# Optimization experiments

Measured on AMD Instinct MI355X. Metric: run time of the kernel, lower is better.

## Reference

```python
import jax, jax.numpy as jnp
import numpy as np

N = 50000
E = 800000
IN_C = 128
HID = 128
OUT_C = 128
EPS = 1e-5


def _glorot(key, shape):
    fan_in = shape[-1]
    return jax.random.normal(key, shape, dtype=jnp.float32) / jnp.sqrt(jnp.float32(fan_in))


def setup_inputs() -> dict:
    key = jax.random.key(0)
    ks = jax.random.split(key, 16)
    inp = {
        'x': jax.random.normal(ks[0], (N, IN_C), dtype=jnp.float32),
        'edge_index': jax.random.randint(ks[1], (2, E), 0, N, dtype=jnp.int64),
    }
    dims = [(IN_C, HID), (HID, HID), (HID, OUT_C)]
    for i, (din, dout) in enumerate(dims, start=1):
        inp[f'Wl{i}'] = _glorot(ks[2 * i], (dout, din))      # applied to aggregated neighbors
        inp[f'bl{i}'] = jnp.zeros((dout,), dtype=jnp.float32)
        inp[f'Wr{i}'] = _glorot(ks[2 * i + 1], (dout, din))  # applied to root node
        inp[f'g{i}'] = jnp.ones((dout,), dtype=jnp.float32)   # BN gamma
        inp[f'b{i}'] = jnp.zeros((dout,), dtype=jnp.float32)  # BN beta
    inp['Wlin'] = _glorot(ks[10], (OUT_C, 2 * HID + OUT_C))
    inp['blin'] = jnp.zeros((OUT_C,), dtype=jnp.float32)
    return inp


def _sage(x, src, dst, Wl, bl, Wr):
    # mean aggregation of source features at target nodes (PyG SAGEConv default)
    msg = x[src]                                              # [E, C]
    s = jax.ops.segment_sum(msg, dst, num_segments=N)         # [N, C]
    cnt = jax.ops.segment_sum(jnp.ones((src.shape[0], 1), x.dtype), dst, num_segments=N)
    aggr = s / jnp.maximum(cnt, 1.0)
    return aggr @ Wl.T + bl + x @ Wr.T


def _bn(x, g, b):
    # training-mode BatchNorm1d over the node dimension
    mu = jnp.mean(x, axis=0)
    var = jnp.var(x, axis=0)
    return g * (x - mu) * jax.lax.rsqrt(var + EPS) + b


def reference(x, edge_index, Wl1, bl1, Wr1, g1, b1, Wl2, bl2, Wr2, g2, b2,
              Wl3, bl3, Wr3, g3, b3, Wlin, blin):
    src, dst = edge_index[0], edge_index[1]
    x1 = _bn(jax.nn.relu(_sage(x, src, dst, Wl1, bl1, Wr1)), g1, b1)
    x2 = _bn(jax.nn.relu(_sage(x1, src, dst, Wl2, bl2, Wr2)), g2, b2)
    x3 = _bn(jax.nn.relu(_sage(x2, src, dst, Wl3, bl3, Wr3)), g3, b3)
    cat = jnp.concatenate([x1, x2, x3], axis=-1)              # [N, 2*HID + OUT_C]
    return jax.nn.relu(cat @ Wlin.T + blin)
```

## Files before the change

### kernel.cpp

```cpp
#include <hip/hip_runtime.h>

#define NN 50000
#define NE 800000
#define CH 128
#define EPSV 1e-5f

typedef unsigned short ushort_t;
typedef __attribute__((ext_vector_type(8))) short short8_t;
typedef __attribute__((ext_vector_type(8))) unsigned short u16x8;
typedef __attribute__((ext_vector_type(4))) float f32x4;

__device__ inline float bf2f(ushort_t u) {
    union { unsigned int i; float f; } t; t.i = ((unsigned int)u) << 16; return t.f;
}
__device__ inline ushort_t f2bf(float f) {
    union { float f; unsigned int i; } t; t.f = f;
    unsigned int r = t.i + 0x7fff + ((t.i >> 16) & 1);
    return (ushort_t)(r >> 16);
}


__global__ void k_hist(const int* __restrict__ dst, int* __restrict__ deg) {
    int e = blockIdx.x * blockDim.x + threadIdx.x;
    if (e < NE) atomicAdd(&deg[dst[e]], 1);
}

__global__ void k_scan(const int* __restrict__ deg, int* __restrict__ row_ptr) {
    __shared__ int wsum[16];
    const int t = threadIdx.x;
    const int lane = t & 63;
    const int wid = t >> 6;
    int carry = 0;
    for (int base = 0; base < NN; base += 1024) {
        int i = base + t;
        int v = (i < NN) ? deg[i] : 0;
        int x = v;
        #pragma unroll
        for (int off = 1; off < 64; off <<= 1) {
            int y = __shfl_up(x, off, 64);
            if (lane >= off) x += y;
        }
        if (lane == 63) wsum[wid] = x;
        __syncthreads();
        if (wid == 0 && lane < 16) {
            int s = wsum[lane];
            #pragma unroll
            for (int off = 1; off < 16; off <<= 1) {
                int y = __shfl_up(s, off, 16);
                if (lane >= off) s += y;
            }
            wsum[lane] = s;
        }
        __syncthreads();
        int wbase = (wid > 0) ? wsum[wid - 1] : 0;
        if (i < NN) row_ptr[i] = carry + wbase + x - v;
        carry += wsum[15];
        __syncthreads();
    }
    if (t == 0) row_ptr[NN] = carry;
}

__global__ void k_fill(const int* __restrict__ src, const int* __restrict__ dst,
                       const int* __restrict__ row_ptr, int* __restrict__ fillc,
                       int* __restrict__ csr) {
    int e = blockIdx.x * blockDim.x + threadIdx.x;
    if (e < NE) {
        int d = dst[e];
        int pos = row_ptr[d] + atomicAdd(&fillc[d], 1);
        csr[pos] = src[e];
    }
}


__global__ __launch_bounds__(256) void k_cvtX(const float* __restrict__ x,
                                              ushort_t* __restrict__ xb) {
    int i = blockIdx.x * 256 + threadIdx.x;
    if (i >= NN * 32) return;
    float4 v = ((const float4*)x)[i];
    ushort4 o;
    o.x = f2bf(v.x); o.y = f2bf(v.y); o.z = f2bf(v.z); o.w = f2bf(v.w);
    ((ushort4*)xb)[i] = o;
}

__global__ __launch_bounds__(256) void k_pack2(const float* __restrict__ s0,
                                               const float* __restrict__ s1,
                                               ushort_t* __restrict__ dst) {
    int t = blockIdx.x * 256 + threadIdx.x;
    if (t >= 128 * 256) return;
    int o = t >> 8, k = t & 255;
    float v = (k < 128) ? s0[o * 128 + k] : s1[o * 128 + k - 128];
    dst[t] = f2bf(v);
}

__global__ void k_packfold(const float* __restrict__ Wl, const float* __restrict__ Wr,
                           const float* __restrict__ ab, const float* __restrict__ bl,
                           ushort_t* __restrict__ Wp, float* __restrict__ bias) {
    __shared__ float red[128];
    int o = blockIdx.x;
    int k = threadIdx.x;
    float wr = Wr[o * 128 + k];
    Wp[o * 256 + k]       = f2bf(Wl[o * 128 + k]);
    Wp[o * 256 + 128 + k] = f2bf(wr * ab[k]);
    red[k] = wr * ab[128 + k];
    __syncthreads();
    for (int s = 64; s > 0; s >>= 1) {
        if (k < s) red[k] += red[k + s];
        __syncthreads();
    }
    if (k == 0) bias[o] = bl[o] + red[0];
}

__global__ void k_packfoldF(const float* __restrict__ Wlin,
                            const float* __restrict__ ab1, const float* __restrict__ ab2,
                            const float* __restrict__ ab3, const float* __restrict__ blin,
                            ushort_t* __restrict__ Wp, float* __restrict__ bias) {
    __shared__ float red[128];
    int o = blockIdx.x;
    int k = threadIdx.x;
    const float* abs_[3] = {ab1, ab2, ab3};
    float dot = 0.f;
    #pragma unroll
    for (int i = 0; i < 3; ++i) {
        float w = Wlin[o * 384 + i * 128 + k];
        Wp[o * 384 + i * 128 + k] = f2bf(w * abs_[i][k]);
        dot += w * abs_[i][128 + k];
    }
    red[k] = dot;
    __syncthreads();
    for (int s = 64; s > 0; s >>= 1) {
        if (k < s) red[k] += red[k + s];
        __syncthreads();
    }
    if (k == 0) bias[o] = blin[o] + red[0];
}


template<bool FOLD>
__global__ __launch_bounds__(256) void k_aggr(const ushort_t* __restrict__ x,
        const int* __restrict__ row_ptr, const int* __restrict__ csr,
        const float* __restrict__ ab, ushort_t* __restrict__ aggr) {
    const int node = blockIdx.x * 4 + (threadIdx.x >> 6);
    const int lane = threadIdx.x & 63;
    const int l4 = lane & 15;
    const int q  = lane >> 4;
    const int r0 = row_ptr[node], r1 = row_ptr[node + 1];
    const int d = r1 - r0;

    float accA[8] = {0, 0, 0, 0, 0, 0, 0, 0};
    float accB[8] = {0, 0, 0, 0, 0, 0, 0, 0};

    int j = r0 + q;
    for (; j + 4 < r1; j += 8) {
        int s0 = csr[j], s1 = csr[j + 4];
        u16x8 v0 = *(const u16x8*)&x[(size_t)s0 * CH + l4 * 8];
        u16x8 v1 = *(const u16x8*)&x[(size_t)s1 * CH + l4 * 8];
        #pragma unroll
        for (int i = 0; i < 8; ++i) {
            accA[i] += bf2f(v0[i]);
            accB[i] += bf2f(v1[i]);
        }
    }
    for (; j < r1; j += 4) {
        int s0 = csr[j];
        u16x8 v0 = *(const u16x8*)&x[(size_t)s0 * CH + l4 * 8];
        #pragma unroll
        for (int i = 0; i < 8; ++i) accA[i] += bf2f(v0[i]);
    }

    const float sc = d > 0 ? 1.0f / (float)d : 0.0f;
    #pragma unroll
    for (int i = 0; i < 8; ++i) {
        float s = accA[i] + accB[i];
        s += __shfl_xor(s, 16);
        s += __shfl_xor(s, 32);
        accA[i] = s * sc;
    }

    if (q == 0) {
        u16x8 ov;
        #pragma unroll
        for (int i = 0; i < 8; ++i) {
            float v = accA[i];
            if (FOLD) v = d > 0 ? fmaf(v, ab[l4 * 8 + i], ab[128 + l4 * 8 + i]) : 0.f;
            ov[i] = f2bf(v);
        }
        *(u16x8*)&aggr[(size_t)node * CH + l4 * 8] = ov;
    }
}


#define STAGE(buf, t) do {                                                           \
    const ushort_t* Ab_ = (((t) >> 1) == 0) ? A0 : ((((t) >> 1) == 1) ? A1 : A2);    \
    Ab_ += ((t) & 1) * 64;                                                           \
    const ushort_t* Wb_ = W + (t) * 64;                                              \
    _Pragma("unroll")                                                                \
    for (int i_ = 0; i_ < 4; ++i_) {                                                 \
        int f_ = i_ * 256 + tid;                                                     \
        int row_ = f_ >> 3;                                                          \
        int c_ = (f_ & 7) ^ (row_ & 7);                                              \
        int gr_ = bn0 + row_; gr_ = gr_ < NN ? gr_ : NN - 1;                         \
        __builtin_amdgcn_global_load_lds(                                            \
            (const __attribute__((address_space(1))) unsigned int*)(Ab_ + (size_t)gr_ * CH + c_ * 8), \
            (__attribute__((address_space(3))) unsigned int*)(&Abuf[buf][f_ * 8]),   \
            16, 0, 0);                                                               \
        __builtin_amdgcn_global_load_lds(                                            \
            (const __attribute__((address_space(1))) unsigned int*)(Wb_ + (size_t)row_ * (NT * 64) + c_ * 8), \
            (__attribute__((address_space(3))) unsigned int*)(&Wbuf[buf][f_ * 8]),   \
            16, 0, 0);                                                               \
    } } while (0)

template<int NT, bool STATS, bool F32OUT>
__global__ __launch_bounds__(256, 2) void k_mgemm(
    const ushort_t* __restrict__ A0, const ushort_t* __restrict__ A1,
    const ushort_t* __restrict__ A2,
    const ushort_t* __restrict__ W, const float* __restrict__ bias,
    ushort_t* __restrict__ outb, float* __restrict__ outf,
    float* __restrict__ bn_sums)
{
    __shared__ __align__(16) ushort_t Abuf[2][128 * 64];
    __shared__ __align__(16) ushort_t Wbuf[2][128 * 64];
    __shared__ float bns[128], bnq[128];

    const int tid  = threadIdx.x;
    const int lane = tid & 63;
    const int wid  = tid >> 6;
    const int l15  = lane & 15;
    const int lg   = lane >> 4;
    const int wn   = (wid >> 1) * 64;
    const int wo   = (wid & 1) * 64;
    const int bn0  = blockIdx.x * 128;

    if (STATS && tid < 128) { bns[tid] = 0.f; bnq[tid] = 0.f; }

    f32x4 acc[4][4];
    #pragma unroll
    for (int i = 0; i < 4; ++i)
        #pragma unroll
        for (int j = 0; j < 4; ++j)
            acc[i][j] = (f32x4){0.f, 0.f, 0.f, 0.f};

    STAGE(0, 0);
    asm volatile("s_waitcnt vmcnt(0)");
    __syncthreads();

    #pragma unroll
    for (int t = 0; t < NT; ++t) {
        const int cur = t & 1;
        if (t + 1 < NT) STAGE(cur ^ 1, t + 1);
        #pragma unroll
        for (int s = 0; s < 2; ++s) {
            short8_t af[4], wf[4];
            #pragma unroll
            for (int b = 0; b < 4; ++b) {
                int ra = wn + b * 16 + l15;
                int ca = (s * 4 + lg) ^ (ra & 7);
                af[b] = *(const short8_t*)&Abuf[cur][ra * 64 + ca * 8];
                int rw = wo + b * 16 + l15;
                int cw = (s * 4 + lg) ^ (rw & 7);
                wf[b] = *(const short8_t*)&Wbuf[cur][rw * 64 + cw * 8];
            }
            #pragma unroll
            for (int i = 0; i < 4; ++i)
                #pragma unroll
                for (int j = 0; j < 4; ++j)
                    acc[i][j] = __builtin_amdgcn_mfma_f32_16x16x32_bf16(
                        af[i], wf[j], acc[i][j], 0, 0, 0);
        }
        asm volatile("s_waitcnt vmcnt(0)");
        __syncthreads();
    }

    float bv[4];
    #pragma unroll
    for (int j = 0; j < 4; ++j) bv[j] = bias[wo + j * 16 + l15];

    float sum[4] = {0.f, 0.f, 0.f, 0.f}, sq[4] = {0.f, 0.f, 0.f, 0.f};

    #pragma unroll
    for (int i = 0; i < 4; ++i) {
        #pragma unroll
        for (int r = 0; r < 4; ++r) {
            int gn = bn0 + wn + i * 16 + lg * 4 + r;
            bool ok = gn < NN;
            #pragma unroll
            for (int j = 0; j < 4; ++j) {
                int o = wo + j * 16 + l15;
                float v = acc[i][j][r] + bv[j];
                v = fmaxf(v, 0.f);
                if (ok) {
                    if (F32OUT) outf[(size_t)gn * CH + o] = v;
                    else        outb[(size_t)gn * CH + o] = f2bf(v);
                    if (STATS) { sum[j] += v; sq[j] += v * v; }
                }
            }
        }
    }

    if (STATS) {
        #pragma unroll
        for (int j = 0; j < 4; ++j) {
            float ss = sum[j], qq = sq[j];
            ss += __shfl_xor(ss, 16); qq += __shfl_xor(qq, 16);
            ss += __shfl_xor(ss, 32); qq += __shfl_xor(qq, 32);
            if (lg == 0) {
                atomicAdd(&bns[wo + j * 16 + l15], ss);
                atomicAdd(&bnq[wo + j * 16 + l15], qq);
            }
        }
        __syncthreads();
        if (tid < 128) {
            atomicAdd(&bn_sums[tid], bns[tid]);
            atomicAdd(&bn_sums[128 + tid], bnq[tid]);
        }
    }
}


__global__ void k_bnfin(const float* __restrict__ bn_sums, const float* __restrict__ g,
                        const float* __restrict__ b, float* __restrict__ ab) {
    int o = threadIdx.x;
    float mu = bn_sums[o] * (1.0f / NN);
    float var = bn_sums[128 + o] * (1.0f / NN) - mu * mu;
    var = var > 0.f ? var : 0.f;
    float rstd = rsqrtf(var + EPSV);
    float a = g[o] * rstd;
    ab[o] = a;
    ab[128 + o] = b[o] - a * mu;
}


extern "C" void kernel_launch(void* const* d_in, const int* in_sizes, int n_in,
                              void* d_out, int out_size, void* d_ws, size_t ws_size,
                              hipStream_t stream) {
    const float* x  = (const float*)d_in[0];
    const int*   ei = (const int*)d_in[1];
    const int* esrc = ei;
    const int* edst = ei + NE;

    const float* Wl[3] = {(const float*)d_in[2],  (const float*)d_in[7],  (const float*)d_in[12]};
    const float* bl[3] = {(const float*)d_in[3],  (const float*)d_in[8],  (const float*)d_in[13]};
    const float* Wr[3] = {(const float*)d_in[4],  (const float*)d_in[9],  (const float*)d_in[14]};
    const float* gg[3] = {(const float*)d_in[5],  (const float*)d_in[10], (const float*)d_in[15]};
    const float* bb[3] = {(const float*)d_in[6],  (const float*)d_in[11], (const float*)d_in[16]};
    const float* Wlin  = (const float*)d_in[17];
    const float* blin  = (const float*)d_in[18];

    float* fo = (float*)d_out;

    const size_t NC = (size_t)NN * CH;
    ushort_t* xb     = (ushort_t*)d_ws;
    ushort_t* y1b    = xb + NC;
    ushort_t* y2b    = y1b + NC;
    ushort_t* y3b    = y2b + NC;
    ushort_t* aggr_b = y3b + NC;
    ushort_t* Wp1    = aggr_b + NC;
    ushort_t* Wp2    = Wp1 + 128 * 256;
    ushort_t* Wp3    = Wp2 + 128 * 256;
    ushort_t* WpF    = Wp3 + 128 * 256;
    float* bias2     = (float*)(WpF + 128 * 384);
    float* bias3     = bias2 + 128;
    float* biasF     = bias3 + 128;
    float* bn_sums   = biasF + 128;
    float* ab        = bn_sums + 768;
    int* row_ptr     = (int*)(ab + 768);
    int* fillc       = row_ptr + NN + 1;
    int* csr         = fillc + NN;

    hipMemsetAsync(fillc, 0, NN * sizeof(int), stream);
    k_hist<<<(NE + 255) / 256, 256, 0, stream>>>(edst, fillc);
    k_scan<<<1, 1024, 0, stream>>>(fillc, row_ptr);
    hipMemsetAsync(fillc, 0, NN * sizeof(int), stream);
    k_fill<<<(NE + 255) / 256, 256, 0, stream>>>(esrc, edst, row_ptr, fillc, csr);

    k_cvtX<<<(NN * 32 + 255) / 256, 256, 0, stream>>>(x, xb);
    k_pack2<<<128, 256, 0, stream>>>(Wl[0], Wr[0], Wp1);
    hipMemsetAsync(bn_sums, 0, 768 * sizeof(float), stream);

    const int GEMM_GRID = (NN + 127) / 128;

    k_aggr<false><<<NN / 4, 256, 0, stream>>>(xb, row_ptr, csr, nullptr, aggr_b);
    k_mgemm<4, true, false><<<GEMM_GRID, 256, 0, stream>>>(
        aggr_b, xb, nullptr, Wp1, bl[0], y1b, nullptr, bn_sums);
    k_bnfin<<<1, 128, 0, stream>>>(bn_sums, gg[0], bb[0], ab);
    k_packfold<<<128, 128, 0, stream>>>(Wl[1], Wr[1], ab, bl[1], Wp2, bias2);

    k_aggr<true><<<NN / 4, 256, 0, stream>>>(y1b, row_ptr, csr, ab, aggr_b);
    k_mgemm<4, true, false><<<GEMM_GRID, 256, 0, stream>>>(
        aggr_b, y1b, nullptr, Wp2, bias2, y2b, nullptr, bn_sums + 256);
    k_bnfin<<<1, 128, 0, stream>>>(bn_sums + 256, gg[1], bb[1], ab + 256);
    k_packfold<<<128, 128, 0, stream>>>(Wl[2], Wr[2], ab + 256, bl[2], Wp3, bias3);

    k_aggr<true><<<NN / 4, 256, 0, stream>>>(y2b, row_ptr, csr, ab + 256, aggr_b);
    k_mgemm<4, true, false><<<GEMM_GRID, 256, 0, stream>>>(
        aggr_b, y2b, nullptr, Wp3, bias3, y3b, nullptr, bn_sums + 512);
    k_bnfin<<<1, 128, 0, stream>>>(bn_sums + 512, gg[2], bb[2], ab + 512);
    k_packfoldF<<<128, 128, 0, stream>>>(Wlin, ab, ab + 256, ab + 512, blin, WpF, biasF);

    k_mgemm<6, false, true><<<GEMM_GRID, 256, 0, stream>>>(
        y1b, y2b, y3b, WpF, biasF, nullptr, fo, nullptr);
}
```

Measured before the change: 373.3 us.

## Fuse neighbor aggregation into SAGE GEMM and partition CSR build passes

Each SAGE layer's mean aggregation is now computed inside the GEMM kernel: 4 threads per node gather neighbor rows straight into LDS, and the MFMA step then runs over the full K=256 without writing and re-reading an aggr buffer in global memory. The CSR histogram and fill kernels are split into 4 passes over destination ranges, which keeps the atomic targets more cache-local. The tradeoff is a large LDS footprint (one block per CU), a gather phase with less memory parallelism per thread than the old wave-per-node scheme, and four times the reads of the edge list.

```diff
diff --git a/kernel.cpp b/kernel.cpp
--- a/kernel.cpp
+++ b/kernel.cpp
@@ -4,6 +4,8 @@
 #define NE 800000
 #define CH 128
 #define EPSV 1e-5f
+#define NPASS 4
+#define PRANGE 12500
 
 typedef unsigned short ushort_t;
 typedef __attribute__((ext_vector_type(8))) short short8_t;
@@ -20,9 +22,13 @@
 }
 
 
-__global__ void k_hist(const int* __restrict__ dst, int* __restrict__ deg) {
-    int e = blockIdx.x * blockDim.x + threadIdx.x;
-    if (e < NE) atomicAdd(&deg[dst[e]], 1);
+__global__ void k_histp(const int* __restrict__ dst, int* __restrict__ deg,
+                        int lo, int hi) {
+    int e = blockIdx.x * 256 + threadIdx.x;
+    if (e < NE) {
+        int d = dst[e];
+        if (d >= lo && d < hi) atomicAdd(&deg[d], 1);
+    }
 }
 
 __global__ void k_scan(const int* __restrict__ deg, int* __restrict__ row_ptr) {
@@ -60,14 +66,17 @@
     if (t == 0) row_ptr[NN] = carry;
 }
 
-__global__ void k_fill(const int* __restrict__ src, const int* __restrict__ dst,
-                       const int* __restrict__ row_ptr, int* __restrict__ fillc,
-                       int* __restrict__ csr) {
-    int e = blockIdx.x * blockDim.x + threadIdx.x;
+__global__ void k_fillp(const int* __restrict__ src, const int* __restrict__ dst,
+                        const int* __restrict__ row_ptr, int* __restrict__ fillc,
+                        int* __restrict__ csr, int lo, int hi) {
+    int e = blockIdx.x * 256 + threadIdx.x;
     if (e < NE) {
         int d = dst[e];
-        int pos = row_ptr[d] + atomicAdd(&fillc[d], 1);
-        csr[pos] = src[e];
+        int s = src[e];
+        if (d >= lo && d < hi) {
+            int pos = row_ptr[d] + atomicAdd(&fillc[d], 1);
+            csr[pos] = s;
+        }
     }
 }
 
@@ -136,55 +145,171 @@
 
 
 template<bool FOLD>
-__global__ __launch_bounds__(256) void k_aggr(const ushort_t* __restrict__ x,
-        const int* __restrict__ row_ptr, const int* __restrict__ csr,
-        const float* __restrict__ ab, ushort_t* __restrict__ aggr) {
-    const int node = blockIdx.x * 4 + (threadIdx.x >> 6);
-    const int lane = threadIdx.x & 63;
-    const int l4 = lane & 15;
-    const int q  = lane >> 4;
-    const int r0 = row_ptr[node], r1 = row_ptr[node + 1];
-    const int d = r1 - r0;
-
-    float accA[8] = {0, 0, 0, 0, 0, 0, 0, 0};
-    float accB[8] = {0, 0, 0, 0, 0, 0, 0, 0};
-
-    int j = r0 + q;
-    for (; j + 4 < r1; j += 8) {
-        int s0 = csr[j], s1 = csr[j + 4];
-        u16x8 v0 = *(const u16x8*)&x[(size_t)s0 * CH + l4 * 8];
-        u16x8 v1 = *(const u16x8*)&x[(size_t)s1 * CH + l4 * 8];
-        #pragma unroll
-        for (int i = 0; i < 8; ++i) {
-            accA[i] += bf2f(v0[i]);
-            accB[i] += bf2f(v1[i]);
-        }
-    }
-    for (; j < r1; j += 4) {
-        int s0 = csr[j];
-        u16x8 v0 = *(const u16x8*)&x[(size_t)s0 * CH + l4 * 8];
-        #pragma unroll
-        for (int i = 0; i < 8; ++i) accA[i] += bf2f(v0[i]);
-    }
-
-    const float sc = d > 0 ? 1.0f / (float)d : 0.0f;
+__global__ __launch_bounds__(512, 1) void k_fused(
+    const ushort_t* __restrict__ xin,
+    const int* __restrict__ row_ptr, const int* __restrict__ csr,
+    const float* __restrict__ ab,
+    const ushort_t* __restrict__ W, const float* __restrict__ bias,
+    ushort_t* __restrict__ out, float* __restrict__ bn_sums)
+{
+    __shared__ __align__(16) ushort_t Abuf[2][128 * 128];
+    __shared__ __align__(16) ushort_t Wbuf[128 * 256];
+    __shared__ float bns[128], bnq[128];
+
+    const int tid = threadIdx.x;
+    const int bn0 = blockIdx.x * 128;
+
+    if (tid < 128) { bns[tid] = 0.f; bnq[tid] = 0.f; }
+
     #pragma unroll
     for (int i = 0; i < 8; ++i) {
-        float s = accA[i] + accB[i];
-        s += __shfl_xor(s, 16);
-        s += __shfl_xor(s, 32);
-        accA[i] = s * sc;
-    }
-
-    if (q == 0) {
-        u16x8 ov;
-        #pragma unroll
-        for (int i = 0; i < 8; ++i) {
-            float v = accA[i];
-            if (FOLD) v = d > 0 ? fmaf(v, ab[l4 * 8 + i], ab[128 + l4 * 8 + i]) : 0.f;
-            ov[i] = f2bf(v);
-        }
-        *(u16x8*)&aggr[(size_t)node * CH + l4 * 8] = ov;
+        int f = i * 512 + tid;
+        int row = f >> 5, sl = f & 31;
+        int ssl = sl ^ (row & 7);
+        __builtin_amdgcn_global_load_lds(
+            (const __attribute__((address_space(1))) unsigned int*)(W + row * 256 + ssl * 8),
+            (__attribute__((address_space(3))) unsigned int*)(&Wbuf[f * 8]), 16, 0, 0);
+    }
+    #pragma unroll
+    for (int i = 0; i < 4; ++i) {
+        int f = i * 512 + tid;
+        int row = f >> 4, sl = f & 15;
+        int ssl = sl ^ (row & 7);
+        int gr = bn0 + row; gr = gr < NN ? gr : NN - 1;
+        __builtin_amdgcn_global_load_lds(
+            (const __attribute__((address_space(1))) unsigned int*)(xin + (size_t)gr * CH + ssl * 8),
+            (__attribute__((address_space(3))) unsigned int*)(&Abuf[1][f * 8]), 16, 0, 0);
+    }
+
+    {
+        int node = bn0 + (tid >> 2);
+        node = node < NN ? node : NN - 1;
+        const int cb = (tid & 3) * 32;
+        const int r0 = row_ptr[node], r1 = row_ptr[node + 1];
+        float ga[32];
+        #pragma unroll
+        for (int c = 0; c < 32; ++c) ga[c] = 0.f;
+        int j = r0;
+        for (; j + 1 < r1; j += 2) {
+            int s0 = csr[j], s1 = csr[j + 1];
+            const u16x8* p0 = (const u16x8*)(xin + (size_t)s0 * CH + cb);
+            const u16x8* p1 = (const u16x8*)(xin + (size_t)s1 * CH + cb);
+            u16x8 va[4], vb[4];
+            #pragma unroll
+            for (int u = 0; u < 4; ++u) { va[u] = p0[u]; vb[u] = p1[u]; }
+            #pragma unroll
+            for (int u = 0; u < 4; ++u)
+                #pragma unroll
+                for (int c = 0; c < 8; ++c)
+                    ga[u * 8 + c] += bf2f(va[u][c]) + bf2f(vb[u][c]);
+        }
+        if (j < r1) {
+            int s0 = csr[j];
+            const u16x8* p0 = (const u16x8*)(xin + (size_t)s0 * CH + cb);
+            u16x8 va[4];
+            #pragma unroll
+            for (int u = 0; u < 4; ++u) va[u] = p0[u];
+            #pragma unroll
+            for (int u = 0; u < 4; ++u)
+                #pragma unroll
+                for (int c = 0; c < 8; ++c)
+                    ga[u * 8 + c] += bf2f(va[u][c]);
+        }
+        const int deg = r1 - r0;
+        const float sc = deg > 0 ? 1.0f / (float)deg : 0.0f;
+        const int row = tid >> 2;
+        #pragma unroll
+        for (int u = 0; u < 4; ++u) {
+            u16x8 ov;
+            #pragma unroll
+            for (int c = 0; c < 8; ++c) {
+                float v = ga[u * 8 + c] * sc;
+                if (FOLD)
+                    v = deg > 0 ? fmaf(v, ab[cb + u * 8 + c], ab[128 + cb + u * 8 + c]) : 0.f;
+                ov[c] = f2bf(v);
+            }
+            int sl = (cb >> 3) + u;
+            *(u16x8*)&Abuf[0][row * 128 + (sl ^ (row & 7)) * 8] = ov;
+        }
+    }
+
+    asm volatile("s_waitcnt vmcnt(0)");
+    __syncthreads();
+
+    const int lane = tid & 63;
+    const int wid  = tid >> 6;
+    const int l15 = lane & 15, lg = lane >> 4;
+    const int wn = (wid >> 2) * 64;
+    const int wo = (wid & 3) * 32;
+
+    f32x4 acc[4][2];
+    #pragma unroll
+    for (int i = 0; i < 4; ++i)
+        #pragma unroll
+        for (int j = 0; j < 2; ++j)
+            acc[i][j] = (f32x4){0.f, 0.f, 0.f, 0.f};
+
+    #pragma unroll
+    for (int s = 0; s < 8; ++s) {
+        const int half = s >> 2, sh = s & 3;
+        short8_t af[4], wf[2];
+        #pragma unroll
+        for (int i = 0; i < 4; ++i) {
+            int r = wn + i * 16 + l15;
+            int sl = (sh * 4 + lg) ^ (r & 7);
+            af[i] = *(const short8_t*)&Abuf[half][r * 128 + sl * 8];
+        }
+        #pragma unroll
+        for (int j = 0; j < 2; ++j) {
+            int r = wo + j * 16 + l15;
+            int sl = (s * 4 + lg) ^ (r & 7);
+            wf[j] = *(const short8_t*)&Wbuf[r * 256 + sl * 8];
+        }
+        #pragma unroll
+        for (int i = 0; i < 4; ++i)
+            #pragma unroll
+            for (int j = 0; j < 2; ++j)
+                acc[i][j] = __builtin_amdgcn_mfma_f32_16x16x32_bf16(
+                    af[i], wf[j], acc[i][j], 0, 0, 0);
+    }
+
+    float bv[2];
+    #pragma unroll
+    for (int j = 0; j < 2; ++j) bv[j] = bias[wo + j * 16 + l15];
+
+    float sum[2] = {0.f, 0.f}, sq[2] = {0.f, 0.f};
+    #pragma unroll
+    for (int i = 0; i < 4; ++i) {
+        #pragma unroll
+        for (int r = 0; r < 4; ++r) {
+            int gn = bn0 + wn + i * 16 + lg * 4 + r;
+            bool ok = gn < NN;
+            #pragma unroll
+            for (int j = 0; j < 2; ++j) {
+                float v = acc[i][j][r] + bv[j];
+                v = fmaxf(v, 0.f);
+                if (ok) {
+                    out[(size_t)gn * CH + wo + j * 16 + l15] = f2bf(v);
+                    sum[j] += v; sq[j] += v * v;
+                }
+            }
+        }
+    }
+
+    #pragma unroll
+    for (int j = 0; j < 2; ++j) {
+        float ss = sum[j], qq = sq[j];
+        ss += __shfl_xor(ss, 16); qq += __shfl_xor(qq, 16);
+        ss += __shfl_xor(ss, 32); qq += __shfl_xor(qq, 32);
+        if (lg == 0) {
+            atomicAdd(&bns[wo + j * 16 + l15], ss);
+            atomicAdd(&bnq[wo + j * 16 + l15], qq);
+        }
+    }
+    __syncthreads();
+    if (tid < 128) {
+        atomicAdd(&bn_sums[tid], bns[tid]);
+        atomicAdd(&bn_sums[128 + tid], bnq[tid]);
     }
 }
 
@@ -209,17 +334,15 @@
             16, 0, 0);                                                               \
     } } while (0)
 
-template<int NT, bool STATS, bool F32OUT>
+template<int NT>
 __global__ __launch_bounds__(256, 2) void k_mgemm(
     const ushort_t* __restrict__ A0, const ushort_t* __restrict__ A1,
     const ushort_t* __restrict__ A2,
     const ushort_t* __restrict__ W, const float* __restrict__ bias,
-    ushort_t* __restrict__ outb, float* __restrict__ outf,
-    float* __restrict__ bn_sums)
+    float* __restrict__ outf)
 {
     __shared__ __align__(16) ushort_t Abuf[2][128 * 64];
     __shared__ __align__(16) ushort_t Wbuf[2][128 * 64];
-    __shared__ float bns[128], bnq[128];
 
     const int tid  = threadIdx.x;
     const int lane = tid & 63;
@@ -230,8 +353,6 @@
     const int wo   = (wid & 1) * 64;
     const int bn0  = blockIdx.x * 128;
 
-    if (STATS && tid < 128) { bns[tid] = 0.f; bnq[tid] = 0.f; }
-
     f32x4 acc[4][4];
     #pragma unroll
     for (int i = 0; i < 4; ++i)
@@ -274,43 +395,18 @@
     #pragma unroll
     for (int j = 0; j < 4; ++j) bv[j] = bias[wo + j * 16 + l15];
 
-    float sum[4] = {0.f, 0.f, 0.f, 0.f}, sq[4] = {0.f, 0.f, 0.f, 0.f};
-
     #pragma unroll
     for (int i = 0; i < 4; ++i) {
         #pragma unroll
         for (int r = 0; r < 4; ++r) {
             int gn = bn0 + wn + i * 16 + lg * 4 + r;
-            bool ok = gn < NN;
-            #pragma unroll
-            for (int j = 0; j < 4; ++j) {
-                int o = wo + j * 16 + l15;
-                float v = acc[i][j][r] + bv[j];
-                v = fmaxf(v, 0.f);
-                if (ok) {
-                    if (F32OUT) outf[(size_t)gn * CH + o] = v;
-                    else        outb[(size_t)gn * CH + o] = f2bf(v);
-                    if (STATS) { sum[j] += v; sq[j] += v * v; }
+            if (gn < NN) {
+                #pragma unroll
+                for (int j = 0; j < 4; ++j) {
+                    float v = acc[i][j][r] + bv[j];
+                    outf[(size_t)gn * CH + wo + j * 16 + l15] = fmaxf(v, 0.f);
                 }
             }
-        }
-    }
-
-    if (STATS) {
-        #pragma unroll
-        for (int j = 0; j < 4; ++j) {
-            float ss = sum[j], qq = sq[j];
-            ss += __shfl_xor(ss, 16); qq += __shfl_xor(qq, 16);
-            ss += __shfl_xor(ss, 32); qq += __shfl_xor(qq, 32);
-            if (lg == 0) {
-                atomicAdd(&bns[wo + j * 16 + l15], ss);
-                atomicAdd(&bnq[wo + j * 16 + l15], qq);
-            }
-        }
-        __syncthreads();
-        if (tid < 128) {
-            atomicAdd(&bn_sums[tid], bns[tid]);
-            atomicAdd(&bn_sums[128 + tid], bnq[tid]);
         }
     }
 }
@@ -348,54 +444,52 @@
     float* fo = (float*)d_out;
 
     const size_t NC = (size_t)NN * CH;
-    ushort_t* xb     = (ushort_t*)d_ws;
-    ushort_t* y1b    = xb + NC;
-    ushort_t* y2b    = y1b + NC;
-    ushort_t* y3b    = y2b + NC;
-    ushort_t* aggr_b = y3b + NC;
-    ushort_t* Wp1    = aggr_b + NC;
-    ushort_t* Wp2    = Wp1 + 128 * 256;
-    ushort_t* Wp3    = Wp2 + 128 * 256;
-    ushort_t* WpF    = Wp3 + 128 * 256;
-    float* bias2     = (float*)(WpF + 128 * 384);
-    float* bias3     = bias2 + 128;
-    float* biasF     = bias3 + 128;
-    float* bn_sums   = biasF + 128;
-    float* ab        = bn_sums + 768;
-    int* row_ptr     = (int*)(ab + 768);
-    int* fillc       = row_ptr + NN + 1;
-    int* csr         = fillc + NN;
+    ushort_t* xb   = (ushort_t*)d_ws;
+    ushort_t* y1b  = xb + NC;
+    ushort_t* y2b  = y1b + NC;
+    ushort_t* y3b  = y2b + NC;
+    ushort_t* Wp1  = y3b + NC;
+    ushort_t* Wp2  = Wp1 + 128 * 256;
+    ushort_t* Wp3  = Wp2 + 128 * 256;
+    ushort_t* WpF  = Wp3 + 128 * 256;
+    float* bias2   = (float*)(WpF + 128 * 384);
+    float* bias3   = bias2 + 128;
+    float* biasF   = bias3 + 128;
+    float* bn_sums = biasF + 128;
+    float* ab      = bn_sums + 768;
+    int* row_ptr   = (int*)(ab + 768);
+    int* fillc     = row_ptr + NN + 1;
+    int* csr       = fillc + NN;
 
     hipMemsetAsync(fillc, 0, NN * sizeof(int), stream);
-    k_hist<<<(NE + 255) / 256, 256, 0, stream>>>(edst, fillc);
+    for (int p = 0; p < NPASS; ++p)
+        k_histp<<<NE / 256, 256, 0, stream>>>(edst, fillc, p * PRANGE, (p + 1) * PRANGE);
     k_scan<<<1, 1024, 0, stream>>>(fillc, row_ptr);
     hipMemsetAsync(fillc, 0, NN * sizeof(int), stream);
-    k_fill<<<(NE + 255) / 256, 256, 0, stream>>>(esrc, edst, row_ptr, fillc, csr);
+    for (int p = 0; p < NPASS; ++p)
+        k_fillp<<<NE / 256, 256, 0, stream>>>(esrc, edst, row_ptr, fillc, csr,
+                                              p * PRANGE, (p + 1) * PRANGE);
 
     k_cvtX<<<(NN * 32 + 255) / 256, 256, 0, stream>>>(x, xb);
     k_pack2<<<128, 256, 0, stream>>>(Wl[0], Wr[0], Wp1);
     hipMemsetAsync(bn_sums, 0, 768 * sizeof(float), stream);
 
-    const int GEMM_GRID = (NN + 127) / 128;
-
-    k_aggr<false><<<NN / 4, 256, 0, stream>>>(xb, row_ptr, csr, nullptr, aggr_b);
-    k_mgemm<4, true, false><<<GEMM_GRID, 256, 0, stream>>>(
-        aggr_b, xb, nullptr, Wp1, bl[0], y1b, nullptr, bn_sums);
+    const int FUSE_GRID = (NN + 127) / 128;
+
+    k_fused<false><<<FUSE_GRID, 512, 0, stream>>>(
+        xb, row_ptr, csr, nullptr, Wp1, bl[0], y1b, bn_sums);
     k_bnfin<<<1, 128, 0, stream>>>(bn_sums, gg[0], bb[0], ab);
     k_packfold<<<128, 128, 0, stream>>>(Wl[1], Wr[1], ab, bl[1], Wp2, bias2);
 
-    k_aggr<true><<<NN / 4, 256, 0, stream>>>(y1b, row_ptr, csr, ab, aggr_b);
-    k_mgemm<4, true, false><<<GEMM_GRID, 256, 0, stream>>>(
-        aggr_b, y1b, nullptr, Wp2, bias2, y2b, nullptr, bn_sums + 256);
+    k_fused<true><<<FUSE_GRID, 512, 0, stream>>>(
+        y1b, row_ptr, csr, ab, Wp2, bias2, y2b, bn_sums + 256);
     k_bnfin<<<1, 128, 0, stream>>>(bn_sums + 256, gg[1], bb[1], ab + 256);
     k_packfold<<<128, 128, 0, stream>>>(Wl[2], Wr[2], ab + 256, bl[2], Wp3, bias3);
 
-    k_aggr<true><<<NN / 4, 256, 0, stream>>>(y2b, row_ptr, csr, ab + 256, aggr_b);
-    k_mgemm<4, true, false><<<GEMM_GRID, 256, 0, stream>>>(
-        aggr_b, y2b, nullptr, Wp3, bias3, y3b, nullptr, bn_sums + 512);
+    k_fused<true><<<FUSE_GRID, 512, 0, stream>>>(
+        y2b, row_ptr, csr, ab + 256, Wp3, bias3, y3b, bn_sums + 512);
     k_bnfin<<<1, 128, 0, stream>>>(bn_sums + 512, gg[2], bb[2], ab + 512);
     k_packfoldF<<<128, 128, 0, stream>>>(Wlin, ab, ab + 256, ab + 512, blin, WpF, biasF);
 
-    k_mgemm<6, false, true><<<GEMM_GRID, 256, 0, stream>>>(
-        y1b, y2b, y3b, WpF, biasF, nullptr, fo, nullptr);
-}
+    k_mgemm<6><<<FUSE_GRID, 256, 0, stream>>>(y1b, y2b, y3b, WpF, biasF, fo);
+}
```

Result: no change. 367.9 us (-1.5%).
